# Performance work log

Hardware: AMD Instinct MI355X
Metric: run time of the kernel (lower is better)

The kernel has to match this reference:

```python
import jax, jax.numpy as jnp
import numpy as np

N, F_IN, HID, LAYERS, HEADS = 50000, 17, 64, 12, 2
E = 400000
EPS_BN = 1e-5


def _bn(x, gamma, beta):
    # BatchNorm1d training-mode forward: batch stats over node dim
    m = x.mean(0)
    v = x.var(0)
    return (x - m) * jax.lax.rsqrt(v + EPS_BN) * gamma + beta


def _gatv2(x, src, dst, Wl, Wr, att, bias):
    # GATv2Conv(hidden, hidden, heads=2, concat=False): mean over heads
    xl = (x @ Wl).reshape(N, HEADS, HID)  # source transform
    xr = (x @ Wr).reshape(N, HEADS, HID)  # target transform
    s = xl[src] + xr[dst]                         # [E,H,C]
    e = (jax.nn.leaky_relu(s, 0.2) * att).sum(-1) # [E,H]
    emax = jax.ops.segment_max(e, dst, num_segments=N)
    emax = jnp.where(jnp.isfinite(emax), emax, 0.0)
    ex = jnp.exp(e - emax[dst])
    denom = jax.ops.segment_sum(ex, dst, num_segments=N)
    alpha = ex / (denom[dst] + 1e-16)             # segment softmax per dst
    msg = (alpha[:, :, None] * xl[src]).reshape(-1, HEADS * HID)
    out = jax.ops.segment_sum(msg, dst, num_segments=N).reshape(N, HEADS, HID)
    return out.mean(1) + bias


def setup_inputs() -> dict:
    key = jax.random.key(0)
    ks = jax.random.split(key, 20)
    d = {}
    d['x'] = jax.random.normal(ks[0], (N, F_IN), dtype=jnp.float32)
    d['edge_index'] = jax.random.randint(ks[1], (2, E), 0, N, dtype=jnp.int32)
    # input projection + BN
    d['in_W'] = jax.random.normal(ks[2], (F_IN, HID), dtype=jnp.float32) * 0.1
    d['in_b'] = jnp.zeros((HID,), jnp.float32)
    d['in_gamma'] = jnp.ones((HID,), jnp.float32)
    d['in_beta'] = jnp.zeros((HID,), jnp.float32)
    # 12 GATv2 layers (stacked params)
    d['Wl'] = jax.random.normal(ks[3], (LAYERS, HID, HEADS * HID), dtype=jnp.float32) * 0.1
    d['Wr'] = jax.random.normal(ks[4], (LAYERS, HID, HEADS * HID), dtype=jnp.float32) * 0.1
    d['att'] = jax.random.normal(ks[5], (LAYERS, HEADS, HID), dtype=jnp.float32) * 0.1
    d['conv_bias'] = jnp.zeros((LAYERS, HID), jnp.float32)
    d['bn_gamma'] = jnp.ones((LAYERS, HID), jnp.float32)
    d['bn_beta'] = jnp.zeros((LAYERS, HID), jnp.float32)
    # output head
    d['out_W1'] = jax.random.normal(ks[6], (HID, 32), dtype=jnp.float32) * 0.1
    d['out_b1'] = jnp.zeros((32,), jnp.float32)
    d['out_W2'] = jax.random.normal(ks[7], (32, 1), dtype=jnp.float32) * 0.1
    d['out_b2'] = jnp.zeros((1,), jnp.float32)
    return d


def reference(x, edge_index, in_W, in_b, in_gamma, in_beta, Wl, Wr, att,
              conv_bias, bn_gamma, bn_beta, out_W1, out_b1, out_W2, out_b2):
    # add self loops (PyG GATv2Conv default add_self_loops=True)
    loops = jnp.arange(N, dtype=edge_index.dtype)
    src = jnp.concatenate([edge_index[0], loops])
    dst = jnp.concatenate([edge_index[1], loops])
    h = jax.nn.elu(_bn(x @ in_W + in_b, in_gamma, in_beta))
    for i in range(LAYERS):
        identity = h
        h = _gatv2(h, src, dst, Wl[i], Wr[i], att[i], conv_bias[i])
        h = jax.nn.elu(_bn(h, bn_gamma[i], bn_beta[i]))
        h = h + identity  # dropout is identity in eval
    h = jax.nn.elu(h @ out_W1 + out_b1)
    h = h @ out_W2 + out_b2
    return jax.nn.sigmoid(h)
```

## Files before the change

### kernel.cpp

```cpp
#include <hip/hip_runtime.h>

#define NN 50000
#define F_IN 17
#define HIDC 64
#define NLAYERS 12
#define NE 400000
#define NET (NE + NN)
#define EPS_BN 1e-5f
#define NREP 8

typedef unsigned short u16;
typedef __bf16 bf16x8 __attribute__((ext_vector_type(8)));
typedef float f32x4 __attribute__((ext_vector_type(4)));

__device__ __forceinline__ float bf2f(u16 v) {
    union { unsigned int i; float f; } u; u.i = ((unsigned int)v) << 16; return u.f;
}
__device__ __forceinline__ u16 f2bf(float f) {
    union { float f; unsigned int i; } u; u.f = f;
    unsigned int r = u.i + 0x7fffu + ((u.i >> 16) & 1u);
    return (u16)(r >> 16);
}
__device__ __forceinline__ float2 bf2x(unsigned int w) {
    union { unsigned int i; float f; } a, b;
    a.i = w << 16; b.i = w & 0xffff0000u;
    float2 r; r.x = a.f; r.y = b.f; return r;
}
__device__ __forceinline__ void unpack8(uint4 w, float* f) {
    float2 a = bf2x(w.x), b = bf2x(w.y), c = bf2x(w.z), d = bf2x(w.w);
    f[0] = a.x; f[1] = a.y; f[2] = b.x; f[3] = b.y;
    f[4] = c.x; f[5] = c.y; f[6] = d.x; f[7] = d.y;
}

__global__ void k_zero_i(int* __restrict__ p, int n) {
    int i = blockIdx.x * blockDim.x + threadIdx.x;
    if (i < n) p[i] = 0;
}
__global__ void k_zero_f(float* __restrict__ p, int n) {
    int i = blockIdx.x * blockDim.x + threadIdx.x;
    if (i < n) p[i] = 0.f;
}

__global__ void k_wt(const float* __restrict__ Wl, const float* __restrict__ Wr,
                     u16* __restrict__ WThi, u16* __restrict__ WTlo) {
    int t = blockIdx.x * blockDim.x + threadIdx.x;
    if (t >= NLAYERS * 256 * HIDC) return;
    int k = t & 63, j = (t >> 6) & 255, i = t >> 14;
    int jj = (j < 128) ? j : (j - 128);
    float v = (j < 128) ? Wl[(i * HIDC + k) * 128 + jj] : Wr[(i * HIDC + k) * 128 + jj];
    u16 hi = f2bf(v);
    u16 lo = f2bf(v - bf2f(hi));
    WThi[t] = hi; WTlo[t] = lo;
}

__global__ void k_count(const int* __restrict__ ei, int* __restrict__ deg) {
    int e = blockIdx.x * blockDim.x + threadIdx.x;
    if (e < NE) {
        int d = ei[NE + e];
        if ((unsigned)d < NN) atomicAdd(&deg[d], 1);
    }
}

__global__ void k_scan1(const int* __restrict__ deg, int* __restrict__ tmp, int* __restrict__ part) {
    __shared__ int s[256];
    int b = blockIdx.x, t = threadIdx.x;
    int n = b * 256 + t;
    int v = (n < NN) ? deg[n] + 1 : 0;
    s[t] = v; __syncthreads();
    for (int o = 1; o < 256; o <<= 1) {
        int a = s[t];
        int w = (t >= o) ? s[t - o] : 0;
        __syncthreads();
        s[t] = a + w;
        __syncthreads();
    }
    if (n < NN) tmp[n] = s[t];
    if (t == 255) part[b] = s[255];
}
__global__ void k_scan2(int* __restrict__ part) {
    __shared__ int s[256];
    int t = threadIdx.x;
    int v = (t < 196) ? part[t] : 0;
    s[t] = v; __syncthreads();
    for (int o = 1; o < 256; o <<= 1) {
        int a = s[t];
        int w = (t >= o) ? s[t - o] : 0;
        __syncthreads();
        s[t] = a + w;
        __syncthreads();
    }
    if (t < 196) part[t] = s[t] - v;
    if (t == 195) part[196] = s[195];
}
__global__ void k_scan3(const int* __restrict__ deg, const int* __restrict__ tmp,
                        const int* __restrict__ part, int* __restrict__ rp, int* __restrict__ cur) {
    int b = blockIdx.x, t = threadIdx.x;
    int n = b * 256 + t;
    if (n < NN) {
        int e = tmp[n] - (deg[n] + 1) + part[b];
        rp[n] = e; cur[n] = e;
    }
    if (n == 0) rp[NN] = part[196];
}

__global__ void k_scatter(const int* __restrict__ ei, int* __restrict__ cur, int* __restrict__ col) {
    int e = blockIdx.x * blockDim.x + threadIdx.x;
    if (e >= NET) return;
    int s, d;
    if (e < NE) { s = ei[e]; d = ei[NE + e]; } else { s = d = e - NE; }
    if ((unsigned)s >= NN) s = 0;
    if ((unsigned)d >= NN) d = 0;
    int p = atomicAdd(&cur[d], 1);
    if ((unsigned)p < NET) col[p] = s;
}

__global__ void k_inproj(const float* __restrict__ x, const float* __restrict__ W, const float* __restrict__ b,
                         float* __restrict__ g, float* __restrict__ bns) {
    __shared__ float ls[64], lq[64];
    int t = threadIdx.x;
    if (t < 64) { ls[t] = 0.f; lq[t] = 0.f; }
    __syncthreads();
    int j = t & 63;
    float wcol[F_IN];
#pragma unroll
    for (int k = 0; k < F_IN; k++) wcol[k] = W[k * 64 + j];
    float bias = b[j];
    float sA = 0.f, sQ = 0.f;
    for (int idx = blockIdx.x * blockDim.x + t; idx < NN * 64; idx += gridDim.x * blockDim.x) {
        int node = idx >> 6;
        float acc = bias;
#pragma unroll
        for (int k = 0; k < F_IN; k++) acc += x[node * F_IN + k] * wcol[k];
        g[idx] = acc;
        sA += acc; sQ += acc * acc;
    }
    atomicAdd(&ls[j], sA); atomicAdd(&lq[j], sQ);
    __syncthreads();
    if (t < 64) atomicAdd(&bns[t], ls[t]);
    else if (t < 128) atomicAdd(&bns[t], lq[t - 64]);
}

#define LDP 72
__global__ __launch_bounds__(256) void k_gemmbn(const float* __restrict__ g, const float* __restrict__ bns,
                                                const float* __restrict__ gamma, const float* __restrict__ beta,
                                                float* h, int residual,
                                                const u16* __restrict__ WThi, const u16* __restrict__ WTlo,
                                                u16* __restrict__ xlxr) {
    __shared__ u16 shi[64 * LDP];
    __shared__ u16 slo[64 * LDP];
    __shared__ float sbn[128];
    int t = threadIdx.x;
    int node0 = blockIdx.x * 64;
    int lane = t & 63, wv = t >> 6;
    int ml = lane & 15, kb = (lane >> 4) * 8;
    if (t < 128) {
        float s = 0.f;
#pragma unroll
        for (int r = 0; r < NREP; r++) s += bns[r * 128 + t];
        sbn[t] = s;
    }
    bf16x8 bh[4][2], bl[4][2];
#pragma unroll
    for (int c = 0; c < 4; c++) {
        int col0 = (wv * 4 + c) * 16;
        size_t brow = (size_t)(col0 + ml) * 64 + kb;
        bh[c][0] = *(const bf16x8*)(WThi + brow);
        bh[c][1] = *(const bf16x8*)(WThi + brow + 32);
        bl[c][0] = *(const bf16x8*)(WTlo + brow);
        bl[c][1] = *(const bf16x8*)(WTlo + brow + 32);
    }
    __syncthreads();
#pragma unroll
    for (int r = 0; r < 4; r++) {
        int nd = r * 16 + (t >> 4);
        int ch = (t & 15) * 4;
        int node = node0 + nd;
        float4 out = {0.f, 0.f, 0.f, 0.f};
        if (node < NN) {
            size_t gpos = (size_t)node * 64 + ch;
            float4 gg = *(const float4*)(g + gpos);
#pragma unroll
            for (int rr = 0; rr < 4; rr++) {
                int c = ch + rr;
                float mean = sbn[c] * (1.0f / NN);
                float var = sbn[64 + c] * (1.0f / NN) - mean * mean;
                var = fmaxf(var, 0.f);
                float rstd = rsqrtf(var + EPS_BN);
                float v = ((&gg.x)[rr] - mean) * rstd * gamma[c] + beta[c];
                (&out.x)[rr] = v > 0.f ? v : (__expf(v) - 1.f);
            }
            if (residual) {
                float4 hh = *(const float4*)(h + gpos);
                out.x += hh.x; out.y += hh.y; out.z += hh.z; out.w += hh.w;
            }
            *(float4*)(h + gpos) = out;
        }
        ushort4 phi, plo;
#pragma unroll
        for (int rr = 0; rr < 4; rr++) {
            float v = (&out.x)[rr];
            u16 hi = f2bf(v);
            u16 lo = f2bf(v - bf2f(hi));
            (&phi.x)[rr] = hi; (&plo.x)[rr] = lo;
        }
        *(ushort4*)(shi + nd * LDP + ch) = phi;
        *(ushort4*)(slo + nd * LDP + ch) = plo;
    }
    __syncthreads();
#pragma unroll
    for (int nt = 0; nt < 4; nt++) {
        int arow = (nt * 16 + ml) * LDP + kb;
        bf16x8 ah0 = *(const bf16x8*)(shi + arow);
        bf16x8 ah1 = *(const bf16x8*)(shi + arow + 32);
        bf16x8 al0 = *(const bf16x8*)(slo + arow);
        bf16x8 al1 = *(const bf16x8*)(slo + arow + 32);
        int rowb = node0 + nt * 16 + (lane >> 4) * 4;
#pragma unroll
        for (int c = 0; c < 4; c++) {
            f32x4 acc = {0.f, 0.f, 0.f, 0.f};
            acc = __builtin_amdgcn_mfma_f32_16x16x32_bf16(al0, bh[c][0], acc, 0, 0, 0);
            acc = __builtin_amdgcn_mfma_f32_16x16x32_bf16(al1, bh[c][1], acc, 0, 0, 0);
            acc = __builtin_amdgcn_mfma_f32_16x16x32_bf16(ah0, bl[c][0], acc, 0, 0, 0);
            acc = __builtin_amdgcn_mfma_f32_16x16x32_bf16(ah1, bl[c][1], acc, 0, 0, 0);
            acc = __builtin_amdgcn_mfma_f32_16x16x32_bf16(ah0, bh[c][0], acc, 0, 0, 0);
            acc = __builtin_amdgcn_mfma_f32_16x16x32_bf16(ah1, bh[c][1], acc, 0, 0, 0);
            int colj = (wv * 4 + c) * 16 + ml;
#pragma unroll
            for (int r = 0; r < 4; r++)
                if (rowb + r < NN) xlxr[(size_t)(rowb + r) * 256 + colj] = f2bf(acc[r]);
        }
    }
}

__global__ __launch_bounds__(256) void k_edge(const uint4* __restrict__ xw4, const int* __restrict__ rp,
                                              const int* __restrict__ col, const float* __restrict__ attL,
                                              const float* __restrict__ cbL, float* __restrict__ g,
                                              float* __restrict__ bns) {
    __shared__ float ls[64], lq[64];
    int t = threadIdx.x;
    if (t < 64) { ls[t] = 0.f; lq[t] = 0.f; }
    __syncthreads();
    int lane = t & 63;
    int q = lane & 15;
    int gsub = lane >> 4;
    int slot = (blockIdx.x * 4 + (t >> 6)) * 4 + gsub;
    int nslot = gridDim.x * 16;
    float atv[8];
#pragma unroll
    for (int i = 0; i < 8; i++) atv[i] = attL[8 * q + i];
    float cbv[8];
#pragma unroll
    for (int i = 0; i < 8; i++) cbv[i] = 0.f;
    if (q < 8) {
#pragma unroll
        for (int i = 0; i < 8; i++) cbv[i] = cbL[8 * q + i];
    }
    float sacc[8], qacc[8];
#pragma unroll
    for (int i = 0; i < 8; i++) { sacc[i] = 0.f; qacc[i] = 0.f; }
    for (int d = slot; d < NN; d += nslot) {
        float xr[8];
        { uint4 w = xw4[(size_t)d * 32 + 16 + q]; unpack8(w, xr); }
        int beg = rp[d], end = rp[d + 1];
        float m = -1e30f, lsum = 0.f;
        float acc[8];
#pragma unroll
        for (int i = 0; i < 8; i++) acc[i] = 0.f;
        int s0 = col[beg];
        uint4 xlw = xw4[(size_t)s0 * 32 + q];
        for (int idx = beg; idx < end; idx++) {
            uint4 curw = xlw;
            if (idx + 1 < end) {
                int s2 = col[idx + 1];
                xlw = xw4[(size_t)s2 * 32 + q];
            }
            float xl[8]; unpack8(curw, xl);
            float p = 0.f;
#pragma unroll
            for (int i = 0; i < 8; i++) {
                float u = xl[i] + xr[i];
                float lr = u > 0.f ? u : 0.2f * u;
                p += lr * atv[i];
            }
            p += __shfl_xor(p, 1); p += __shfl_xor(p, 2); p += __shfl_xor(p, 4);
            float mn = fmaxf(m, p);
            float sc = __expf(m - mn);
            float pw = __expf(p - mn);
            lsum = lsum * sc + pw;
#pragma unroll
            for (int i = 0; i < 8; i++) acc[i] = acc[i] * sc + pw * xl[i];
            m = mn;
        }
        float inv = 1.0f / (lsum + 1e-16f);
#pragma unroll
        for (int i = 0; i < 8; i++) {
            float v = acc[i] * inv;
            acc[i] = 0.5f * (v + __shfl_xor(v, 8));
        }
        if (q < 8) {
            float4 w0, w1;
#pragma unroll
            for (int i = 0; i < 8; i++) {
                float c = acc[i] + cbv[i];
                sacc[i] += c; qacc[i] += c * c;
                if (i < 4) (&w0.x)[i] = c; else (&w1.x)[i - 4] = c;
            }
            *(float4*)(g + (size_t)d * 64 + 8 * q) = w0;
            *(float4*)(g + (size_t)d * 64 + 8 * q + 4) = w1;
        }
    }
    if (q < 8) {
#pragma unroll
        for (int i = 0; i < 8; i++) {
            atomicAdd(&ls[8 * q + i], sacc[i]);
            atomicAdd(&lq[8 * q + i], qacc[i]);
        }
    }
    __syncthreads();
    float* bb = bns + (blockIdx.x & (NREP - 1)) * 128;
    if (t < 64) atomicAdd(&bb[t], ls[t]);
    else if (t < 128) atomicAdd(&bb[t], lq[t - 64]);
}

__global__ void k_fold(const float* __restrict__ bns, float* __restrict__ bout) {
    int t = threadIdx.x;
    if (t < 128) {
        float s = 0.f;
#pragma unroll
        for (int r = 0; r < NREP; r++) s += bns[r * 128 + t];
        bout[t] = s;
    }
}

__global__ void k_bnfinal(const float* __restrict__ g, const float* __restrict__ bns,
                          const float* __restrict__ gamma, const float* __restrict__ beta, float* h) {
    int t = blockIdx.x * blockDim.x + threadIdx.x;
    if (t >= NN * 16) return;
    int c4 = (t & 15) * 4;
    float4 gg = *(const float4*)(g + (size_t)t * 4);
    float4 out;
#pragma unroll
    for (int r = 0; r < 4; r++) {
        int c = c4 + r;
        float mean = bns[c] * (1.0f / NN);
        float var = bns[64 + c] * (1.0f / NN) - mean * mean;
        var = fmaxf(var, 0.f);
        float rstd = rsqrtf(var + EPS_BN);
        float v = ((&gg.x)[r] - mean) * rstd * gamma[c] + beta[c];
        (&out.x)[r] = v > 0.f ? v : (__expf(v) - 1.f);
    }
    float4 hh = *(const float4*)(h + (size_t)t * 4);
    out.x += hh.x; out.y += hh.y; out.z += hh.z; out.w += hh.w;
    *(float4*)(h + (size_t)t * 4) = out;
}

__global__ void k_head(const float* __restrict__ h, const float* __restrict__ W1, const float* __restrict__ b1,
                       const float* __restrict__ W2, const float* __restrict__ b2, float* __restrict__ out) {
    int t = blockIdx.x * blockDim.x + threadIdx.x;
    int node = t >> 5;
    int j = t & 31;
    if (node >= NN) return;
    float acc = b1[j];
    const float* hr = h + (size_t)node * 64;
#pragma unroll
    for (int k = 0; k < 64; k++) acc += hr[k] * W1[k * 32 + j];
    float e = acc > 0.f ? acc : (__expf(acc) - 1.f);
    float z = e * W2[j];
    z += __shfl_xor(z, 1); z += __shfl_xor(z, 2); z += __shfl_xor(z, 4);
    z += __shfl_xor(z, 8); z += __shfl_xor(z, 16);
    if (j == 0) {
        float y = z + b2[0];
        out[node] = 1.0f / (1.0f + __expf(-y));
    }
}

extern "C" void kernel_launch(void* const* d_in, const int* in_sizes, int n_in,
                              void* d_out, int out_size, void* d_ws, size_t ws_size,
                              hipStream_t stream) {
    const float* x = (const float*)d_in[0];
    const int* ei = (const int*)d_in[1];
    const float* inW = (const float*)d_in[2];
    const float* inb = (const float*)d_in[3];
    const float* ing = (const float*)d_in[4];
    const float* inbeta = (const float*)d_in[5];
    const float* Wl = (const float*)d_in[6];
    const float* Wr = (const float*)d_in[7];
    const float* att = (const float*)d_in[8];
    const float* cb = (const float*)d_in[9];
    const float* bng = (const float*)d_in[10];
    const float* bnb = (const float*)d_in[11];
    const float* W1 = (const float*)d_in[12];
    const float* b1 = (const float*)d_in[13];
    const float* W2 = (const float*)d_in[14];
    const float* b2 = (const float*)d_in[15];
    float* out = (float*)d_out;

    char* ws = (char*)d_ws;
    size_t off = 0;
    auto alloc = [&](size_t bytes) -> char* {
        char* p = ws + off;
        off = (off + bytes + 255) & ~(size_t)255;
        return p;
    };
    float* h    = (float*)alloc((size_t)NN * 64 * 4);
    float* g    = (float*)alloc((size_t)NN * 64 * 4);
    u16* xlxr   = (u16*)alloc((size_t)NN * 256 * 2);
    u16* WThi   = (u16*)alloc((size_t)NLAYERS * 256 * 64 * 2);
    u16* WTlo   = (u16*)alloc((size_t)NLAYERS * 256 * 64 * 2);
    int* deg    = (int*)alloc((size_t)NN * 4);
    int* rp     = (int*)alloc((size_t)(NN + 1) * 4);
    int* cur    = (int*)alloc((size_t)NN * 4);
    int* colv   = (int*)alloc((size_t)NET * 4);
    int* stmp   = (int*)alloc((size_t)NN * 4);
    int* part   = (int*)alloc(256 * 4);
    float* bns  = (float*)alloc((size_t)(NLAYERS + 1) * NREP * 128 * 4);
    float* bnsf = (float*)alloc(128 * 4);

    k_zero_i<<<(NN + 255) / 256, 256, 0, stream>>>(deg, NN);
    k_zero_f<<<((NLAYERS + 1) * NREP * 128 + 255) / 256, 256, 0, stream>>>(bns, (NLAYERS + 1) * NREP * 128);

    k_wt<<<(NLAYERS * 256 * HIDC + 255) / 256, 256, 0, stream>>>(Wl, Wr, WThi, WTlo);
    k_count<<<(NE + 255) / 256, 256, 0, stream>>>(ei, deg);
    k_scan1<<<196, 256, 0, stream>>>(deg, stmp, part);
    k_scan2<<<1, 256, 0, stream>>>(part);
    k_scan3<<<196, 256, 0, stream>>>(deg, stmp, part, rp, cur);
    k_scatter<<<(NET + 255) / 256, 256, 0, stream>>>(ei, cur, colv);

    k_inproj<<<512, 256, 0, stream>>>(x, inW, inb, g, bns);

    for (int i = 0; i < NLAYERS; i++) {
        const float* gamma = (i == 0) ? ing : bng + (size_t)(i - 1) * 64;
        const float* beta  = (i == 0) ? inbeta : bnb + (size_t)(i - 1) * 64;
        k_gemmbn<<<782, 256, 0, stream>>>(g, bns + (size_t)i * NREP * 128, gamma, beta, h, (i > 0) ? 1 : 0,
                                          WThi + (size_t)i * 16384, WTlo + (size_t)i * 16384, xlxr);
        k_edge<<<1563, 256, 0, stream>>>((const uint4*)xlxr, rp, colv,
                                         att + (size_t)i * 128, cb + (size_t)i * 64,
                                         g, bns + (size_t)(i + 1) * NREP * 128);
    }
    k_fold<<<1, 128, 0, stream>>>(bns + (size_t)NLAYERS * NREP * 128, bnsf);
    k_bnfinal<<<3125, 256, 0, stream>>>(g, bnsf,
                                        bng + (size_t)(NLAYERS - 1) * 64, bnb + (size_t)(NLAYERS - 1) * 64, h);
    k_head<<<6250, 256, 0, stream>>>(h, W1, b1, W2, b2, out);
}
```

Measured before the change: 1.066 ms.

## Split xl/xr into separate buffers and fuse final BN, residual and head

The interleaved xl|xr bf16 buffer becomes two contiguous 128-wide arrays, so the gather of source xl rows in the edge kernel touches a denser 25.6 MB array and packs fewer unused xr bytes into each cache line. The final fold, BN/ELU/residual and output-head kernels are merged into one tail kernel that keeps the per-node hidden vector in shared memory, removing two launches and one round trip of h through global memory. Every block now redoes the small NREP fold, which is cheap.

```diff
diff --git a/kernel.cpp b/kernel.cpp
--- a/kernel.cpp
+++ b/kernel.cpp
@@ -145,7 +145,7 @@
                                                 const float* __restrict__ gamma, const float* __restrict__ beta,
                                                 float* h, int residual,
                                                 const u16* __restrict__ WThi, const u16* __restrict__ WTlo,
-                                                u16* __restrict__ xlxr) {
+                                                u16* __restrict__ xlb, u16* __restrict__ xrb) {
     __shared__ u16 shi[64 * LDP];
     __shared__ u16 slo[64 * LDP];
     __shared__ float sbn[128];
@@ -227,12 +227,17 @@
             int colj = (wv * 4 + c) * 16 + ml;
 #pragma unroll
             for (int r = 0; r < 4; r++)
-                if (rowb + r < NN) xlxr[(size_t)(rowb + r) * 256 + colj] = f2bf(acc[r]);
-        }
-    }
-}
-
-__global__ __launch_bounds__(256) void k_edge(const uint4* __restrict__ xw4, const int* __restrict__ rp,
+                if (rowb + r < NN) {
+                    u16 v = f2bf(acc[r]);
+                    if (colj < 128) xlb[(size_t)(rowb + r) * 128 + colj] = v;
+                    else xrb[(size_t)(rowb + r) * 128 + (colj - 128)] = v;
+                }
+        }
+    }
+}
+
+__global__ __launch_bounds__(256) void k_edge(const uint4* __restrict__ xl4, const uint4* __restrict__ xr4,
+                                              const int* __restrict__ rp,
                                               const int* __restrict__ col, const float* __restrict__ attL,
                                               const float* __restrict__ cbL, float* __restrict__ g,
                                               float* __restrict__ bns) {
@@ -260,19 +265,19 @@
     for (int i = 0; i < 8; i++) { sacc[i] = 0.f; qacc[i] = 0.f; }
     for (int d = slot; d < NN; d += nslot) {
         float xr[8];
-        { uint4 w = xw4[(size_t)d * 32 + 16 + q]; unpack8(w, xr); }
+        { uint4 w = xr4[(size_t)d * 16 + q]; unpack8(w, xr); }
         int beg = rp[d], end = rp[d + 1];
         float m = -1e30f, lsum = 0.f;
         float acc[8];
 #pragma unroll
         for (int i = 0; i < 8; i++) acc[i] = 0.f;
         int s0 = col[beg];
-        uint4 xlw = xw4[(size_t)s0 * 32 + q];
+        uint4 xlw = xl4[(size_t)s0 * 16 + q];
         for (int idx = beg; idx < end; idx++) {
             uint4 curw = xlw;
             if (idx + 1 < end) {
                 int s2 = col[idx + 1];
-                xlw = xw4[(size_t)s2 * 32 + q];
+                xlw = xl4[(size_t)s2 * 16 + q];
             }
             float xl[8]; unpack8(curw, xl);
             float p = 0.f;
@@ -322,46 +327,44 @@
     else if (t < 128) atomicAdd(&bb[t], lq[t - 64]);
 }
 
-__global__ void k_fold(const float* __restrict__ bns, float* __restrict__ bout) {
+__global__ __launch_bounds__(256) void k_tail(const float* __restrict__ g, const float* __restrict__ bns,
+                                              const float* __restrict__ gamma, const float* __restrict__ beta,
+                                              const float* __restrict__ h,
+                                              const float* __restrict__ W1, const float* __restrict__ b1,
+                                              const float* __restrict__ W2, const float* __restrict__ b2,
+                                              float* __restrict__ out) {
+    __shared__ float sbn[128];
+    __shared__ float sh[8 * 64];
     int t = threadIdx.x;
     if (t < 128) {
         float s = 0.f;
 #pragma unroll
         for (int r = 0; r < NREP; r++) s += bns[r * 128 + t];
-        bout[t] = s;
-    }
-}
-
-__global__ void k_bnfinal(const float* __restrict__ g, const float* __restrict__ bns,
-                          const float* __restrict__ gamma, const float* __restrict__ beta, float* h) {
-    int t = blockIdx.x * blockDim.x + threadIdx.x;
-    if (t >= NN * 16) return;
-    int c4 = (t & 15) * 4;
-    float4 gg = *(const float4*)(g + (size_t)t * 4);
-    float4 out;
-#pragma unroll
-    for (int r = 0; r < 4; r++) {
-        int c = c4 + r;
-        float mean = bns[c] * (1.0f / NN);
-        float var = bns[64 + c] * (1.0f / NN) - mean * mean;
-        var = fmaxf(var, 0.f);
-        float rstd = rsqrtf(var + EPS_BN);
-        float v = ((&gg.x)[r] - mean) * rstd * gamma[c] + beta[c];
-        (&out.x)[r] = v > 0.f ? v : (__expf(v) - 1.f);
-    }
-    float4 hh = *(const float4*)(h + (size_t)t * 4);
-    out.x += hh.x; out.y += hh.y; out.z += hh.z; out.w += hh.w;
-    *(float4*)(h + (size_t)t * 4) = out;
-}
-
-__global__ void k_head(const float* __restrict__ h, const float* __restrict__ W1, const float* __restrict__ b1,
-                       const float* __restrict__ W2, const float* __restrict__ b2, float* __restrict__ out) {
-    int t = blockIdx.x * blockDim.x + threadIdx.x;
-    int node = t >> 5;
+        sbn[t] = s;
+    }
+    __syncthreads();
+    int nl = t >> 5;
     int j = t & 31;
+    int node = blockIdx.x * 8 + nl;
+    if (node < NN) {
+#pragma unroll
+        for (int half = 0; half < 2; half++) {
+            int c = j + half * 32;
+            float mean = sbn[c] * (1.0f / NN);
+            float var = sbn[64 + c] * (1.0f / NN) - mean * mean;
+            var = fmaxf(var, 0.f);
+            float rstd = rsqrtf(var + EPS_BN);
+            float gg = g[(size_t)node * 64 + c];
+            float v = (gg - mean) * rstd * gamma[c] + beta[c];
+            v = v > 0.f ? v : (__expf(v) - 1.f);
+            v += h[(size_t)node * 64 + c];
+            sh[nl * 64 + c] = v;
+        }
+    }
+    __syncthreads();
     if (node >= NN) return;
     float acc = b1[j];
-    const float* hr = h + (size_t)node * 64;
+    const float* hr = sh + nl * 64;
 #pragma unroll
     for (int k = 0; k < 64; k++) acc += hr[k] * W1[k * 32 + j];
     float e = acc > 0.f ? acc : (__expf(acc) - 1.f);
@@ -404,7 +407,8 @@
     };
     float* h    = (float*)alloc((size_t)NN * 64 * 4);
     float* g    = (float*)alloc((size_t)NN * 64 * 4);
-    u16* xlxr   = (u16*)alloc((size_t)NN * 256 * 2);
+    u16* xlb    = (u16*)alloc((size_t)NN * 128 * 2);
+    u16* xrb    = (u16*)alloc((size_t)NN * 128 * 2);
     u16* WThi   = (u16*)alloc((size_t)NLAYERS * 256 * 64 * 2);
     u16* WTlo   = (u16*)alloc((size_t)NLAYERS * 256 * 64 * 2);
     int* deg    = (int*)alloc((size_t)NN * 4);
@@ -414,7 +418,6 @@
     int* stmp   = (int*)alloc((size_t)NN * 4);
     int* part   = (int*)alloc(256 * 4);
     float* bns  = (float*)alloc((size_t)(NLAYERS + 1) * NREP * 128 * 4);
-    float* bnsf = (float*)alloc(128 * 4);
 
     k_zero_i<<<(NN + 255) / 256, 256, 0, stream>>>(deg, NN);
     k_zero_f<<<((NLAYERS + 1) * NREP * 128 + 255) / 256, 256, 0, stream>>>(bns, (NLAYERS + 1) * NREP * 128);
@@ -432,13 +435,12 @@
         const float* gamma = (i == 0) ? ing : bng + (size_t)(i - 1) * 64;
         const float* beta  = (i == 0) ? inbeta : bnb + (size_t)(i - 1) * 64;
         k_gemmbn<<<782, 256, 0, stream>>>(g, bns + (size_t)i * NREP * 128, gamma, beta, h, (i > 0) ? 1 : 0,
-                                          WThi + (size_t)i * 16384, WTlo + (size_t)i * 16384, xlxr);
-        k_edge<<<1563, 256, 0, stream>>>((const uint4*)xlxr, rp, colv,
+                                          WThi + (size_t)i * 16384, WTlo + (size_t)i * 16384, xlb, xrb);
+        k_edge<<<1563, 256, 0, stream>>>((const uint4*)xlb, (const uint4*)xrb, rp, colv,
                                          att + (size_t)i * 128, cb + (size_t)i * 64,
                                          g, bns + (size_t)(i + 1) * NREP * 128);
     }
-    k_fold<<<1, 128, 0, stream>>>(bns + (size_t)NLAYERS * NREP * 128, bnsf);
-    k_bnfinal<<<3125, 256, 0, stream>>>(g, bnsf,
-                                        bng + (size_t)(NLAYERS - 1) * 64, bnb + (size_t)(NLAYERS - 1) * 64, h);
-    k_head<<<6250, 256, 0, stream>>>(h, W1, b1, W2, b2, out);
-}
+    k_tail<<<6250, 256, 0, stream>>>(g, bns + (size_t)NLAYERS * NREP * 128,
+                                     bng + (size_t)(NLAYERS - 1) * 64, bnb + (size_t)(NLAYERS - 1) * 64,
+                                     h, W1, b1, W2, b2, out);
+}
```

Result: no change. 1.068 ms (median of 2 runs) (+0.2%).
